# Kernel tuning notes

Hardware: AMD Instinct MI355X
Metric: run time of the kernel (lower is better)

## Reference

```python
import jax, jax.numpy as jnp
import numpy as np

N = 100000
E = 3200000
F_IN = 128
H = 64
B = 128


def _sage(x, edge_index, Wl, bl, Wr):
    # PyG SAGEConv (aggr='mean'): out = lin_l(mean_{j in N(i)} x_j) + lin_r(x_i)
    src, dst = edge_index[0], edge_index[1]
    msg = x[src]                                            # [E, F] gather
    agg = jax.ops.segment_sum(msg, dst, num_segments=x.shape[0])
    cnt = jax.ops.segment_sum(jnp.ones((edge_index.shape[1],), x.dtype), dst,
                              num_segments=x.shape[0])
    mean = agg / jnp.maximum(cnt, 1.0)[:, None]
    return mean @ Wl + bl + x @ Wr


def _encode(x, edge_index, batch, p1, p2, num_graphs):
    h = jax.nn.relu(_sage(x, edge_index, *p1))
    h = jax.nn.relu(_sage(h, edge_index, *p2))
    # global_mean_pool
    s = jax.ops.segment_sum(h, batch, num_segments=num_graphs)
    c = jax.ops.segment_sum(jnp.ones((h.shape[0],), h.dtype), batch,
                            num_segments=num_graphs)
    return s / jnp.maximum(c, 1.0)[:, None]


def setup_inputs() -> dict:
    key = jax.random.key(0)
    ks = jax.random.split(key, 20)
    inp = {
        "state_x": jax.random.normal(ks[0], (N, F_IN), dtype=jnp.float32),
        "state_edge_index": jax.random.randint(ks[1], (2, E), 0, N),
        "state_batch": jnp.sort(jax.random.randint(ks[2], (N,), 0, B)),
        "goal_x": jax.random.normal(ks[3], (N, F_IN), dtype=jnp.float32),
        "goal_edge_index": jax.random.randint(ks[4], (2, E), 0, N),
        "goal_batch": jnp.sort(jax.random.randint(ks[5], (N,), 0, B)),
        "depth": jax.random.uniform(ks[6], (B, 1), dtype=jnp.float32) * 20.0,
    }
    def lin(k, fin, fout):
        s = 1.0 / np.sqrt(fin)
        return jax.random.uniform(k, (fin, fout), minval=-s, maxval=s, dtype=jnp.float32)
    # SAGEConv params: Wl (neighbor, with bias), Wr (root, no bias)
    names = ["s1", "s2", "g1", "g2"]
    fins = [F_IN, H, F_IN, H]
    for i, (nm, fin) in enumerate(zip(names, fins)):
        inp[nm + "_Wl"] = lin(ks[7 + 3 * i], fin, H)
        inp[nm + "_bl"] = jnp.zeros((H,), jnp.float32)
        inp[nm + "_Wr"] = lin(ks[8 + 3 * i], fin, H)
    inp["mlp_W1"] = lin(ks[19], 2 * H + 1, H)
    inp["mlp_b1"] = jnp.zeros((H,), jnp.float32)
    inp["mlp_W2"] = lin(jax.random.fold_in(key, 99), H, 1)
    inp["mlp_b2"] = jnp.zeros((1,), jnp.float32)
    return inp


def reference(state_x, state_edge_index, state_batch,
              goal_x, goal_edge_index, goal_batch, depth,
              s1_Wl, s1_bl, s1_Wr, s2_Wl, s2_bl, s2_Wr,
              g1_Wl, g1_bl, g1_Wr, g2_Wl, g2_bl, g2_Wr,
              mlp_W1, mlp_b1, mlp_W2, mlp_b2):
    state_emb = _encode(state_x, state_edge_index, state_batch,
                        (s1_Wl, s1_bl, s1_Wr), (s2_Wl, s2_bl, s2_Wr), B)
    goal_emb = _encode(goal_x, goal_edge_index, goal_batch,
                       (g1_Wl, g1_bl, g1_Wr), (g2_Wl, g2_bl, g2_Wr), B)
    graph_emb = jnp.concatenate([state_emb, goal_emb], axis=1)   # [B, 2H]
    d_mean = depth.mean()
    d_std = depth.std()  # unbiased=False matches jnp default
    d = (depth - d_mean) / (d_std + 1e-6)
    features = jnp.concatenate([graph_emb, d], axis=1)           # [B, 2H+1]
    h = jax.nn.relu(features @ mlp_W1 + mlp_b1)
    out = h @ mlp_W2 + mlp_b2                                    # [B, 1]
    return out[:, 0]
```

## Files before the change

### kernel.cpp

```cpp
#include <hip/hip_runtime.h>
#include <hip/hip_bf16.h>


#define NB    128
#define EPB   16384
#define BWMAX 1024
#define PP    8
#define SRCB  17


__global__ __launch_bounds__(256) void p1_hist(const int* __restrict__ dstS,
                                               const int* __restrict__ dstG,
                                               int* __restrict__ blkhist,
                                               int E, int bsh, int nblk) {
    const int g = blockIdx.x / nblk;
    const int blk = blockIdx.x % nblk;
    const int* __restrict__ dst = g ? dstG : dstS;
    __shared__ int h[NB];
    for (int i = threadIdx.x; i < NB; i += 256) h[i] = 0;
    __syncthreads();
    const int base = blk * EPB;
    for (int k = 0; k < EPB; k += 256) {
        const int e = base + k + threadIdx.x;
        if (e < E) atomicAdd(&h[dst[e] >> bsh], 1);
    }
    __syncthreads();
    for (int i = threadIdx.x; i < NB; i += 256)
        blkhist[((size_t)(g * nblk + blk)) * NB + i] = h[i];
}

__global__ __launch_bounds__(NB) void p1_scan(const int* __restrict__ blkhist,
                                              int* __restrict__ basem,
                                              int* __restrict__ bucket_base,
                                              int nblk) {
    __shared__ int lds[NB];
    const int g = blockIdx.x;
    const int* __restrict__ bh = blkhist + (size_t)g * nblk * NB;
    int* __restrict__ bm = basem + (size_t)g * nblk * NB;
    int* __restrict__ bb = bucket_base + (size_t)g * (NB + 1);
    const int b = threadIdx.x;
    int s = 0;
    int k = 0;
    for (; k + 8 <= nblk; k += 8) {
        int v[8];
        #pragma unroll
        for (int t = 0; t < 8; ++t) v[t] = bh[(size_t)(k + t) * NB + b];
        #pragma unroll
        for (int t = 0; t < 8; ++t) s += v[t];
    }
    for (; k < nblk; ++k) s += bh[(size_t)k * NB + b];
    lds[b] = s;
    __syncthreads();
    for (int off = 1; off < NB; off <<= 1) {
        int v = (b >= off) ? lds[b - off] : 0;
        __syncthreads();
        lds[b] += v;
        __syncthreads();
    }
    int run = lds[b] - s;
    bb[b] = run;
    if (b == NB - 1) bb[NB] = run + s;
    k = 0;
    for (; k + 8 <= nblk; k += 8) {
        int c[8];
        #pragma unroll
        for (int t = 0; t < 8; ++t) c[t] = bh[(size_t)(k + t) * NB + b];
        #pragma unroll
        for (int t = 0; t < 8; ++t) {
            bm[(size_t)(k + t) * NB + b] = run;
            run += c[t];
        }
    }
    for (; k < nblk; ++k) {
        const int c = bh[(size_t)k * NB + b];
        bm[(size_t)k * NB + b] = run;
        run += c;
    }
}

__global__ __launch_bounds__(256) void p1_scatter(const int* __restrict__ eiS,
                                                  const int* __restrict__ eiG,
                                                  const int* __restrict__ basem,
                                                  int* __restrict__ pairs,
                                                  int E, int bsh, int nblk) {
    const int g = blockIdx.x / nblk;
    const int blk = blockIdx.x % nblk;
    const int* __restrict__ src = g ? eiG : eiS;
    const int* __restrict__ dst = src + E;
    int* __restrict__ pr = pairs + (size_t)g * E;
    const int bwm = (1 << bsh) - 1;
    __shared__ int cur[NB];
    for (int i = threadIdx.x; i < NB; i += 256)
        cur[i] = basem[((size_t)(g * nblk + blk)) * NB + i];
    __syncthreads();
    const int base = blk * EPB;
    for (int k = 0; k < EPB; k += 256) {
        const int e = base + k + threadIdx.x;
        if (e < E) {
            const int d = dst[e];
            const int s = src[e];
            const int p = atomicAdd(&cur[d >> bsh], 1);
            pr[p] = s | ((d & bwm) << SRCB);
        }
    }
}

__global__ __launch_bounds__(512) void p2_sort(const int* __restrict__ pairs,
                                               const int* __restrict__ bucket_base,
                                               int* __restrict__ csr,
                                               int* __restrict__ row_start,
                                               int N, int E, int bsh) {
    __shared__ int cnt[BWMAX];
    __shared__ int off[BWMAX];
    const int g = blockIdx.x / NB;
    const int b = blockIdx.x % NB;
    const int bw = 1 << bsh;
    const int lo = b * bw;
    int nn = N - lo;
    if (nn <= 0) return;
    if (nn > bw) nn = bw;
    const int* __restrict__ pr = pairs + (size_t)g * E;
    const int* __restrict__ bb = bucket_base + (size_t)g * (NB + 1);
    int* __restrict__ cs = csr + (size_t)g * E;
    int* __restrict__ rs = row_start + (size_t)g * (N + 1);
    const int tid = threadIdx.x;
    for (int i = tid; i < nn; i += 512) cnt[i] = 0;
    __syncthreads();
    const int e0 = bb[b];
    const int e1 = bb[b + 1];
    for (int e = e0 + tid; e < e1; e += 512)
        atomicAdd(&cnt[pr[e] >> SRCB], 1);
    __syncthreads();
    if (tid == 0) {
        int run = e0;
        for (int i = 0; i < nn; ++i) { off[i] = run; run += cnt[i]; }
    }
    __syncthreads();
    for (int i = tid; i < nn; i += 512) {
        rs[lo + i] = off[i];
        cnt[i] = off[i];
    }
    if (lo + nn == N && tid == 0) rs[N] = e1;
    __syncthreads();
    for (int e = e0 + tid; e < e1; e += 512) {
        const int v = pr[e];
        const int pos = atomicAdd(&cnt[v >> SRCB], 1);
        cs[pos] = v & ((1 << SRCB) - 1);
    }
}

template <int K>
__global__ __launch_bounds__(512) void gemm_fused(const float* __restrict__ x,
                                                  const float* __restrict__ Wl,
                                                  const float* __restrict__ Wr,
                                                  __hip_bfloat16* __restrict__ Y,
                                                  float* __restrict__ R, int n) {
    constexpr int KC = 64;
    constexpr int ROWS = 64;
    __shared__ float4 ldsW[(KC / 2) * 64];
    __shared__ float  ldsX[ROWS * KC];
    const int tid = threadIdx.x;
    const int lane = tid & 63;
    const int wid = tid >> 6;
    const int rbase = blockIdx.x * ROWS;

    float accY[8], accR[8];
    #pragma unroll
    for (int r = 0; r < 8; ++r) { accY[r] = 0.f; accR[r] = 0.f; }

    for (int k0 = 0; k0 < K; k0 += KC) {
        __syncthreads();
        for (int i = tid; i < (KC / 2) * 64; i += 512) {
            const int k2 = i >> 6;
            const int col = i & 63;
            const int ka = k0 + k2 * 2;
            ldsW[i] = make_float4(Wl[(size_t)ka * 64 + col], Wr[(size_t)ka * 64 + col],
                                  Wl[(size_t)(ka + 1) * 64 + col], Wr[(size_t)(ka + 1) * 64 + col]);
        }
        {
            constexpr int F4R = KC / 4;
            float4* lx = (float4*)ldsX;
            for (int i = tid; i < ROWS * F4R; i += 512) {
                const int rr = i / F4R;
                const int cc = i % F4R;
                int row = rbase + rr;
                if (row > n - 1) row = n - 1;
                lx[i] = *(const float4*)(x + (size_t)row * K + k0 + cc * 4);
            }
        }
        __syncthreads();
        const int rw = wid * 8;
        #pragma unroll 2
        for (int k4 = 0; k4 < KC / 4; ++k4) {
            const float4 wA = ldsW[(k4 * 2 + 0) * 64 + lane];
            const float4 wB = ldsW[(k4 * 2 + 1) * 64 + lane];
            #pragma unroll
            for (int r = 0; r < 8; ++r) {
                const float4 xv = *(const float4*)(&ldsX[(rw + r) * KC + k4 * 4]);
                float y = accY[r];
                float z = accR[r];
                y = fmaf(xv.x, wA.x, y);
                z = fmaf(xv.x, wA.y, z);
                y = fmaf(xv.y, wA.z, y);
                z = fmaf(xv.y, wA.w, z);
                y = fmaf(xv.z, wB.x, y);
                z = fmaf(xv.z, wB.y, z);
                y = fmaf(xv.w, wB.z, y);
                z = fmaf(xv.w, wB.w, z);
                accY[r] = y;
                accR[r] = z;
            }
        }
    }
    #pragma unroll
    for (int r = 0; r < 8; ++r) {
        const int row = rbase + wid * 8 + r;
        if (row < n) {
            Y[(size_t)row * 64 + lane] = __float2bfloat16(accY[r]);
            R[(size_t)row * 64 + lane] = accR[r];
        }
    }
}

__global__ __launch_bounds__(256) void agg_fused(const __hip_bfloat16* __restrict__ Y,
                                                 const float* __restrict__ R,
                                                 const float* __restrict__ bl,
                                                 const int* __restrict__ csr,
                                                 const int* __restrict__ row_start,
                                                 float* __restrict__ H, int n) {
    const int wid = threadIdx.x >> 6;
    const int lane = threadIdx.x & 63;
    const int i = blockIdx.x * 4 + wid;
    if (i >= n) return;
    const int r0 = __builtin_amdgcn_readfirstlane(row_start[i]);
    const int r1 = __builtin_amdgcn_readfirstlane(row_start[i + 1]);
    float a[32];
    #pragma unroll
    for (int t = 0; t < 32; ++t) a[t] = 0.f;
    int e = r0;
    for (; e + 32 <= r1; e += 32) {
        #pragma unroll
        for (int t = 0; t < 32; ++t)
            a[t] += __bfloat162float(Y[(size_t)csr[e + t] * 64 + lane]);
    }
    for (; e + 8 <= r1; e += 8) {
        #pragma unroll
        for (int t = 0; t < 8; ++t)
            a[t] += __bfloat162float(Y[(size_t)csr[e + t] * 64 + lane]);
    }
    for (; e < r1; ++e) a[0] += __bfloat162float(Y[(size_t)csr[e] * 64 + lane]);
    float acc = 0.f;
    #pragma unroll
    for (int t = 0; t < 32; ++t) acc += a[t];
    const int c = r1 - r0;
    const float sc = (c > 0) ? (1.0f / (float)c) : 1.0f;
    const float v = acc * sc + bl[lane] + R[(size_t)i * 64 + lane];
    H[(size_t)i * 64 + lane] = fmaxf(v, 0.0f);
}

__global__ __launch_bounds__(256) void pool_part(const float* __restrict__ H,
                                                 const int* __restrict__ batch,
                                                 float* __restrict__ parts,
                                                 int* __restrict__ pcnt, int n) {
    const int b = blockIdx.x / PP;
    const int p = blockIdx.x % PP;
    int lo = 0, hi = n;
    while (lo < hi) { int m = (lo + hi) >> 1; if (batch[m] < b) lo = m + 1; else hi = m; }
    const int beg = lo;
    hi = n;
    while (lo < hi) { int m = (lo + hi) >> 1; if (batch[m] < b + 1) lo = m + 1; else hi = m; }
    const int end = lo;
    const int len = end - beg;
    const int chunk = (len + PP - 1) / PP;
    const int s0 = beg + p * chunk;
    int s1 = s0 + chunk; if (s1 > end) s1 = end;

    const int wid = threadIdx.x >> 6;
    const int lane = threadIdx.x & 63;
    float acc = 0.f;
    for (int i = s0 + wid; i < s1; i += 4)
        acc += H[(size_t)i * 64 + lane];
    __shared__ float part[4][64];
    part[wid][lane] = acc;
    __syncthreads();
    if (wid == 0) {
        const float s = (part[0][lane] + part[1][lane]) + (part[2][lane] + part[3][lane]);
        parts[(size_t)(b * PP + p) * 64 + lane] = s;
        if (lane == 0 && p == 0) pcnt[b] = len;
    }
}

__global__ __launch_bounds__(128) void final_mlp(const float* __restrict__ partsS,
                                                 const int* __restrict__ cntS,
                                                 const float* __restrict__ partsG,
                                                 const int* __restrict__ cntG,
                                                 const float* __restrict__ depth,
                                                 const float* __restrict__ W1,
                                                 const float* __restrict__ b1,
                                                 const float* __restrict__ W2,
                                                 const float* __restrict__ b2,
                                                 float* __restrict__ out, int Bn) {
    __shared__ float lW1[129 * 64];
    __shared__ float red[128];
    const int t = threadIdx.x;
    for (int i = t; i < 129 * 64; i += 128) lW1[i] = W1[i];
    const float d = (t < Bn) ? depth[t] : 0.0f;
    red[t] = d;
    __syncthreads();
    for (int off = 64; off > 0; off >>= 1) {
        if (t < off) red[t] += red[t + off];
        __syncthreads();
    }
    const float mean = red[0] / (float)Bn;
    __syncthreads();
    const float dev = d - mean;
    red[t] = (t < Bn) ? dev * dev : 0.0f;
    __syncthreads();
    for (int off = 64; off > 0; off >>= 1) {
        if (t < off) red[t] += red[t + off];
        __syncthreads();
    }
    const float stdv = sqrtf(red[0] / (float)Bn);
    const float dn = dev / (stdv + 1e-6f);
    if (t >= Bn) return;

    float acc[64];
    #pragma unroll
    for (int j = 0; j < 64; ++j) acc[j] = b1[j];
    int cs = cntS[t]; if (cs < 1) cs = 1;
    int cg = cntG[t]; if (cg < 1) cg = 1;
    const float invS = 1.0f / (float)cs;
    const float invG = 1.0f / (float)cg;
    for (int k = 0; k < 64; ++k) {
        float fk = 0.f;
        #pragma unroll
        for (int p = 0; p < PP; ++p) fk += partsS[(size_t)(t * PP + p) * 64 + k];
        fk *= invS;
        #pragma unroll
        for (int j = 0; j < 64; ++j) acc[j] = fmaf(fk, lW1[k * 64 + j], acc[j]);
    }
    for (int k = 0; k < 64; ++k) {
        float fk = 0.f;
        #pragma unroll
        for (int p = 0; p < PP; ++p) fk += partsG[(size_t)(t * PP + p) * 64 + k];
        fk *= invG;
        #pragma unroll
        for (int j = 0; j < 64; ++j) acc[j] = fmaf(fk, lW1[(64 + k) * 64 + j], acc[j]);
    }
    #pragma unroll
    for (int j = 0; j < 64; ++j) acc[j] = fmaf(dn, lW1[128 * 64 + j], acc[j]);
    float o = b2[0];
    #pragma unroll
    for (int j = 0; j < 64; ++j) o = fmaf(fmaxf(acc[j], 0.0f), W2[j], o);
    out[t] = o;
}

extern "C" void kernel_launch(void* const* d_in, const int* in_sizes, int n_in,
                              void* d_out, int out_size, void* d_ws, size_t ws_size,
                              hipStream_t stream) {
    const float* state_x     = (const float*)d_in[0];
    const int*   state_ei    = (const int*)d_in[1];
    const int*   state_batch = (const int*)d_in[2];
    const float* goal_x      = (const float*)d_in[3];
    const int*   goal_ei     = (const int*)d_in[4];
    const int*   goal_batch  = (const int*)d_in[5];
    const float* depth       = (const float*)d_in[6];
    const float* s1_Wl = (const float*)d_in[7];
    const float* s1_bl = (const float*)d_in[8];
    const float* s1_Wr = (const float*)d_in[9];
    const float* s2_Wl = (const float*)d_in[10];
    const float* s2_bl = (const float*)d_in[11];
    const float* s2_Wr = (const float*)d_in[12];
    const float* g1_Wl = (const float*)d_in[13];
    const float* g1_bl = (const float*)d_in[14];
    const float* g1_Wr = (const float*)d_in[15];
    const float* g2_Wl = (const float*)d_in[16];
    const float* g2_bl = (const float*)d_in[17];
    const float* g2_Wr = (const float*)d_in[18];
    const float* mlp_W1 = (const float*)d_in[19];
    const float* mlp_b1 = (const float*)d_in[20];
    const float* mlp_W2 = (const float*)d_in[21];
    const float* mlp_b2 = (const float*)d_in[22];

    const int N  = in_sizes[0] / 128;
    const int E  = in_sizes[1] / 2;
    const int Bn = in_sizes[6];
    const int nblk = (E + EPB - 1) / EPB;
    int bsh = 0;
    while (((size_t)NB << bsh) < (size_t)N) ++bsh;

    char* w = (char*)d_ws;
    auto alloc = [&](size_t bytes) {
        char* p = w;
        w += (bytes + 255) & ~(size_t)255;
        return p;
    };
    char*  bufYraw     = alloc((size_t)N * 64 * sizeof(float));
    float* bufR        = (float*)alloc((size_t)N * 64 * sizeof(float));
    float* bufH        = (float*)alloc((size_t)N * 64 * sizeof(float));
    int*   csr         = (int*)alloc((size_t)2 * E * sizeof(int));
    int*   row_start   = (int*)alloc((size_t)2 * (N + 1) * sizeof(int));
    int*   blkhist     = (int*)alloc((size_t)2 * nblk * NB * sizeof(int));
    int*   basem       = (int*)alloc((size_t)2 * nblk * NB * sizeof(int));
    int*   bucket_base = (int*)alloc((size_t)2 * (NB + 1) * sizeof(int));
    float* partsS      = (float*)alloc((size_t)Bn * PP * 64 * sizeof(float));
    float* partsG      = (float*)alloc((size_t)Bn * PP * 64 * sizeof(float));
    int*   cntS        = (int*)alloc((size_t)Bn * sizeof(int));
    int*   cntG        = (int*)alloc((size_t)Bn * sizeof(int));
    __hip_bfloat16* bufY = (__hip_bfloat16*)bufYraw;
    int*   pairs       = (int*)bufYraw;
    const size_t need = (size_t)(w - (char*)d_ws);
    const bool pairs_fit = (size_t)2 * E * sizeof(int) <= (size_t)N * 64 * sizeof(float);
    if (need > ws_size || (1 << bsh) > BWMAX || !pairs_fit || N > (1 << SRCB)) {
        hipMemsetAsync(d_out, 0, (size_t)out_size * sizeof(float), stream);
        return;
    }

    p1_hist<<<2 * nblk, 256, 0, stream>>>(state_ei + E, goal_ei + E, blkhist, E, bsh, nblk);
    p1_scan<<<2, NB, 0, stream>>>(blkhist, basem, bucket_base, nblk);
    p1_scatter<<<2 * nblk, 256, 0, stream>>>(state_ei, goal_ei, basem, pairs, E, bsh, nblk);
    p2_sort<<<2 * NB, 512, 0, stream>>>(pairs, bucket_base, csr, row_start, N, E, bsh);

    const int g64 = (N + 63) / 64;
    const int g4  = (N + 3) / 4;
    const int* csrS = csr;
    const int* csrG = csr + E;
    const int* rsS  = row_start;
    const int* rsG  = row_start + (N + 1);

    gemm_fused<128><<<g64, 512, 0, stream>>>(state_x, s1_Wl, s1_Wr, bufY, bufR, N);
    agg_fused<<<g4, 256, 0, stream>>>(bufY, bufR, s1_bl, csrS, rsS, bufH, N);
    gemm_fused<64><<<g64, 512, 0, stream>>>(bufH, s2_Wl, s2_Wr, bufY, bufR, N);
    agg_fused<<<g4, 256, 0, stream>>>(bufY, bufR, s2_bl, csrS, rsS, bufH, N);
    pool_part<<<Bn * PP, 256, 0, stream>>>(bufH, state_batch, partsS, cntS, N);

    gemm_fused<128><<<g64, 512, 0, stream>>>(goal_x, g1_Wl, g1_Wr, bufY, bufR, N);
    agg_fused<<<g4, 256, 0, stream>>>(bufY, bufR, g1_bl, csrG, rsG, bufH, N);
    gemm_fused<64><<<g64, 512, 0, stream>>>(bufH, g2_Wl, g2_Wr, bufY, bufR, N);
    agg_fused<<<g4, 256, 0, stream>>>(bufY, bufR, g2_bl, csrG, rsG, bufH, N);
    pool_part<<<Bn * PP, 256, 0, stream>>>(bufH, goal_batch, partsG, cntG, N);

    final_mlp<<<1, 128, 0, stream>>>(partsS, cntS, partsG, cntG, depth,
                                     mlp_W1, mlp_b1, mlp_W2, mlp_b2, (float*)d_out, Bn);
}
```

Baseline: 718.0 us.

## Parallelize CSR sort prefix scan, stage scatter in LDS, split final MLP per graph

In the CSR bucket sort, the serial single-thread prefix over up to 1024 counters becomes a 512-thread Hillis-Steele scan. The scattered per-edge stores are staged in shared memory when the bucket fits, then written out contiguously. The final MLP moves from one 128-thread block, which loaded all of W1 into LDS and ran 64 accumulators per thread, to one 64-thread block per graph with wave shuffles for the reductions. The 112 KB stage buffer cuts p2_sort occupancy to one block per CU, and every MLP block recomputes the depth statistics.

```diff
diff --git a/kernel.cpp b/kernel.cpp
--- a/kernel.cpp
+++ b/kernel.cpp
@@ -7,6 +7,7 @@
 #define BWMAX 1024
 #define PP    8
 #define SRCB  17
+#define SCAP  28672
 
 
 __global__ __launch_bounds__(256) void p1_hist(const int* __restrict__ dstS,
@@ -110,8 +111,10 @@
                                                int* __restrict__ csr,
                                                int* __restrict__ row_start,
                                                int N, int E, int bsh) {
+    __shared__ int stage[SCAP];
     __shared__ int cnt[BWMAX];
     __shared__ int off[BWMAX];
+    __shared__ int ws[512];
     const int g = blockIdx.x / NB;
     const int b = blockIdx.x % NB;
     const int bw = 1 << bsh;
@@ -128,12 +131,26 @@
     __syncthreads();
     const int e0 = bb[b];
     const int e1 = bb[b + 1];
+    const int ne = e1 - e0;
     for (int e = e0 + tid; e < e1; e += 512)
         atomicAdd(&cnt[pr[e] >> SRCB], 1);
     __syncthreads();
-    if (tid == 0) {
-        int run = e0;
-        for (int i = 0; i < nn; ++i) { off[i] = run; run += cnt[i]; }
+    {
+        const int i0 = 2 * tid, i1 = 2 * tid + 1;
+        const int c0 = (i0 < nn) ? cnt[i0] : 0;
+        const int c1 = (i1 < nn) ? cnt[i1] : 0;
+        const int s = c0 + c1;
+        ws[tid] = s;
+        __syncthreads();
+        for (int o = 1; o < 512; o <<= 1) {
+            int v = (tid >= o) ? ws[tid - o] : 0;
+            __syncthreads();
+            ws[tid] += v;
+            __syncthreads();
+        }
+        const int base = e0 + ws[tid] - s;
+        if (i0 < nn) off[i0] = base;
+        if (i1 < nn) off[i1] = base + c0;
     }
     __syncthreads();
     for (int i = tid; i < nn; i += 512) {
@@ -142,10 +159,20 @@
     }
     if (lo + nn == N && tid == 0) rs[N] = e1;
     __syncthreads();
-    for (int e = e0 + tid; e < e1; e += 512) {
-        const int v = pr[e];
-        const int pos = atomicAdd(&cnt[v >> SRCB], 1);
-        cs[pos] = v & ((1 << SRCB) - 1);
+    if (ne <= SCAP) {
+        for (int e = e0 + tid; e < e1; e += 512) {
+            const int v = pr[e];
+            const int pos = atomicAdd(&cnt[v >> SRCB], 1);
+            stage[pos - e0] = v & ((1 << SRCB) - 1);
+        }
+        __syncthreads();
+        for (int i = tid; i < ne; i += 512) cs[e0 + i] = stage[i];
+    } else {
+        for (int e = e0 + tid; e < e1; e += 512) {
+            const int v = pr[e];
+            const int pos = atomicAdd(&cnt[v >> SRCB], 1);
+            cs[pos] = v & ((1 << SRCB) - 1);
+        }
     }
 }
 
@@ -290,69 +317,53 @@
     }
 }
 
-__global__ __launch_bounds__(128) void final_mlp(const float* __restrict__ partsS,
-                                                 const int* __restrict__ cntS,
-                                                 const float* __restrict__ partsG,
-                                                 const int* __restrict__ cntG,
-                                                 const float* __restrict__ depth,
-                                                 const float* __restrict__ W1,
-                                                 const float* __restrict__ b1,
-                                                 const float* __restrict__ W2,
-                                                 const float* __restrict__ b2,
-                                                 float* __restrict__ out, int Bn) {
-    __shared__ float lW1[129 * 64];
-    __shared__ float red[128];
-    const int t = threadIdx.x;
-    for (int i = t; i < 129 * 64; i += 128) lW1[i] = W1[i];
-    const float d = (t < Bn) ? depth[t] : 0.0f;
-    red[t] = d;
-    __syncthreads();
-    for (int off = 64; off > 0; off >>= 1) {
-        if (t < off) red[t] += red[t + off];
-        __syncthreads();
-    }
-    const float mean = red[0] / (float)Bn;
-    __syncthreads();
-    const float dev = d - mean;
-    red[t] = (t < Bn) ? dev * dev : 0.0f;
-    __syncthreads();
-    for (int off = 64; off > 0; off >>= 1) {
-        if (t < off) red[t] += red[t + off];
-        __syncthreads();
-    }
-    const float stdv = sqrtf(red[0] / (float)Bn);
-    const float dn = dev / (stdv + 1e-6f);
-    if (t >= Bn) return;
-
-    float acc[64];
-    #pragma unroll
-    for (int j = 0; j < 64; ++j) acc[j] = b1[j];
-    int cs = cntS[t]; if (cs < 1) cs = 1;
-    int cg = cntG[t]; if (cg < 1) cg = 1;
-    const float invS = 1.0f / (float)cs;
-    const float invG = 1.0f / (float)cg;
-    for (int k = 0; k < 64; ++k) {
-        float fk = 0.f;
-        #pragma unroll
-        for (int p = 0; p < PP; ++p) fk += partsS[(size_t)(t * PP + p) * 64 + k];
-        fk *= invS;
-        #pragma unroll
-        for (int j = 0; j < 64; ++j) acc[j] = fmaf(fk, lW1[k * 64 + j], acc[j]);
-    }
-    for (int k = 0; k < 64; ++k) {
-        float fk = 0.f;
-        #pragma unroll
-        for (int p = 0; p < PP; ++p) fk += partsG[(size_t)(t * PP + p) * 64 + k];
-        fk *= invG;
-        #pragma unroll
-        for (int j = 0; j < 64; ++j) acc[j] = fmaf(fk, lW1[(64 + k) * 64 + j], acc[j]);
-    }
-    #pragma unroll
-    for (int j = 0; j < 64; ++j) acc[j] = fmaf(dn, lW1[128 * 64 + j], acc[j]);
-    float o = b2[0];
-    #pragma unroll
-    for (int j = 0; j < 64; ++j) o = fmaf(fmaxf(acc[j], 0.0f), W2[j], o);
-    out[t] = o;
+__global__ __launch_bounds__(64) void final_mlp(const float* __restrict__ partsS,
+                                                const int* __restrict__ cntS,
+                                                const float* __restrict__ partsG,
+                                                const int* __restrict__ cntG,
+                                                const float* __restrict__ depth,
+                                                const float* __restrict__ W1,
+                                                const float* __restrict__ b1,
+                                                const float* __restrict__ W2,
+                                                const float* __restrict__ b2,
+                                                float* __restrict__ out, int Bn) {
+    const int b = blockIdx.x;
+    const int j = threadIdx.x;
+    float dsum = 0.f;
+    for (int i = j; i < Bn; i += 64) dsum += depth[i];
+    #pragma unroll
+    for (int o = 32; o > 0; o >>= 1) dsum += __shfl_xor(dsum, o);
+    const float mean = dsum / (float)Bn;
+    float dvar = 0.f;
+    for (int i = j; i < Bn; i += 64) { const float t = depth[i] - mean; dvar = fmaf(t, t, dvar); }
+    #pragma unroll
+    for (int o = 32; o > 0; o >>= 1) dvar += __shfl_xor(dvar, o);
+    const float stdv = sqrtf(dvar / (float)Bn);
+    const float dn = (depth[b] - mean) / (stdv + 1e-6f);
+
+    __shared__ float f[129];
+    {
+        float s = 0.f, g = 0.f;
+        #pragma unroll
+        for (int p = 0; p < PP; ++p) {
+            s += partsS[(size_t)(b * PP + p) * 64 + j];
+            g += partsG[(size_t)(b * PP + p) * 64 + j];
+        }
+        int cs = cntS[b]; if (cs < 1) cs = 1;
+        int cg = cntG[b]; if (cg < 1) cg = 1;
+        f[j] = s / (float)cs;
+        f[64 + j] = g / (float)cg;
+        if (j == 0) f[128] = dn;
+    }
+    __syncthreads();
+    float acc = b1[j];
+    #pragma unroll 8
+    for (int k = 0; k < 129; ++k)
+        acc = fmaf(f[k], W1[(size_t)k * 64 + j], acc);
+    float o = fmaxf(acc, 0.0f) * W2[j];
+    #pragma unroll
+    for (int of = 32; of > 0; of >>= 1) o += __shfl_xor(o, of);
+    if (j == 0) out[b] = o + b2[0];
 }
 
 extern "C" void kernel_launch(void* const* d_in, const int* in_sizes, int n_in,
@@ -440,6 +451,6 @@
     agg_fused<<<g4, 256, 0, stream>>>(bufY, bufR, g2_bl, csrG, rsG, bufH, N);
     pool_part<<<Bn * PP, 256, 0, stream>>>(bufH, goal_batch, partsG, cntG, N);
 
-    final_mlp<<<1, 128, 0, stream>>>(partsS, cntS, partsG, cntG, depth,
+    final_mlp<<<Bn, 64, 0, stream>>>(partsS, cntS, partsG, cntG, depth,
                                      mlp_W1, mlp_b1, mlp_W2, mlp_b2, (float*)d_out, Bn);
 }
```

After: 660.2 us. 8.0% less time.
